# Kernel optimization log

Measured on AMD Instinct MI355X. Metric: run time of the kernel, lower is better.

Reference implementation:

```python
import jax, jax.numpy as jnp
import numpy as np

BATCH, IN_F, OUT_F = 65536, 1024, 256


def setup_inputs() -> dict:
    key = jax.random.key(0)
    kx, kw, kb, ks = jax.random.split(key, 4)
    x = jax.random.normal(kx, (BATCH, IN_F), dtype=jnp.float32)
    # ternary weight in {-1, 0, 1}, shape [out, in] as in F.linear
    weight = jax.random.randint(kw, (OUT_F, IN_F), -1, 2).astype(jnp.float32)
    # bias is integer-valued (floor'd in get_sign_bias_from_bn)
    bias = jax.random.randint(kb, (OUT_F,), -64, 64).astype(jnp.float32)
    # sign in {-1, +1}, broadcast shape [1, out]
    sign = (jax.random.randint(ks, (1, OUT_F), 0, 2).astype(jnp.float32) * 2.0 - 1.0)
    return {"x": x, "weight": weight, "bias": bias, "sign": sign}


def reference(x, weight, bias, sign):
    # y = F.linear(x, W, b); rounding=True -> round; then threshold by sign
    y = jnp.round(jnp.dot(x, weight.T) + bias)  # [B, out]
    return jnp.where(y * sign >= 0, jnp.float32(1.0), jnp.float32(0.0)).astype(x.dtype)
```

## Files before the change

### kernel.cpp

```cpp
#include <hip/hip_runtime.h>
#include <hip/hip_bf16.h>

#define M_BATCH 65536
#define K_IN    1024
#define N_OUT   256
#define TAU     0.015f

#define XLO_SOFF 67108864ULL
#define WT_SOFF  134217728ULL
#define CNT_BOFF 268959744ULL
#define WL_BOFF  (CNT_BOFF + 256ULL)
#define WL_CAP   1048576ULL
#define WS_NEED  (WL_BOFF + WL_CAP * 4ULL)

typedef __attribute__((ext_vector_type(8))) short short8;
typedef __attribute__((ext_vector_type(4))) short short4v;
typedef __attribute__((ext_vector_type(4))) float f32x4;

__device__ inline short f2bf(float f) {
    __hip_bfloat16 h = __float2bfloat16(f);
    return __builtin_bit_cast(short, h);
}
__device__ inline float bf2f(short s) {
    unsigned u = ((unsigned)(unsigned short)s) << 16;
    return __builtin_bit_cast(float, u);
}
__device__ inline void gload16(const void* g, void* lds) {
    __builtin_amdgcn_global_load_lds(
        (const __attribute__((address_space(1))) unsigned int*)g,
        (__attribute__((address_space(3))) unsigned int*)lds, 16, 0, 0);
}

__device__ inline float c3_score(const float* __restrict__ xr_,
                                 const float* __restrict__ wr_) {
    float a0 = 0.f, a1 = 0.f;
    float4 xc0 = *(const float4*)(xr_);
    float4 wc0 = *(const float4*)(wr_);
    float4 xc1 = *(const float4*)(xr_ + 512);
    float4 wc1 = *(const float4*)(wr_ + 512);
    for (int k4 = 0; k4 < 128; ++k4) {
        const int kn = (k4 + 1) & 127;
        const float4 nx0 = *(const float4*)(xr_ + kn * 4);
        const float4 nw0 = *(const float4*)(wr_ + kn * 4);
        const float4 nx1 = *(const float4*)(xr_ + 512 + kn * 4);
        const float4 nw1 = *(const float4*)(wr_ + 512 + kn * 4);
        a0 = fmaf(xc0.x, wc0.x, a0); a1 = fmaf(xc1.x, wc1.x, a1);
        a0 = fmaf(xc0.y, wc0.y, a0); a1 = fmaf(xc1.y, wc1.y, a1);
        a0 = fmaf(xc0.z, wc0.z, a0); a1 = fmaf(xc1.z, wc1.z, a1);
        a0 = fmaf(xc0.w, wc0.w, a0); a1 = fmaf(xc1.w, wc1.w, a1);
        xc0 = nx0; wc0 = nw0; xc1 = nx1; wc1 = nw1;
    }
    return a0 + a1;
}

__device__ inline size_t swz_dst(int row, int col4 ) {
    const int kb = col4 >> 4;
    const int c  = (col4 >> 1) & 7;
    const int h  = col4 & 1;
    return (size_t)row * K_IN + kb * 64 + ((c ^ (row & 7)) << 3) + h * 4;
}

__global__ __launch_bounds__(512) void presplit20(const float* __restrict__ x,
                                                  short* __restrict__ xhi,
                                                  short* __restrict__ xlo) {
    const int stride = gridDim.x * 512;
    for (int idx = blockIdx.x * 512 + threadIdx.x; idx < M_BATCH * (K_IN / 4); idx += stride) {
        const int row  = idx >> 8;
        const int col4 = idx & 255;
        const float4 v = ((const float4*)x)[idx];
        short4v h, l;
        h.x = f2bf(v.x); l.x = f2bf(v.x - bf2f(h.x));
        h.y = f2bf(v.y); l.y = f2bf(v.y - bf2f(h.y));
        h.z = f2bf(v.z); l.z = f2bf(v.z - bf2f(h.z));
        h.w = f2bf(v.w); l.w = f2bf(v.w - bf2f(h.w));
        const size_t dst = swz_dst(row, col4);
        *(short4v*)(xhi + dst) = h;
        *(short4v*)(xlo + dst) = l;
    }
}

__global__ __launch_bounds__(512) void wconv20(const float* __restrict__ w,
                                               short* __restrict__ wt,
                                               unsigned* __restrict__ counter) {
    if (blockIdx.x == 0 && threadIdx.x == 0) *counter = 0u;
    const int idx  = blockIdx.x * 512 + threadIdx.x;
    const int row  = idx >> 8;
    const int col4 = idx & 255;
    const float4 v = ((const float4*)w)[idx];
    short4v h;
    h.x = f2bf(v.x); h.y = f2bf(v.y); h.z = f2bf(v.z); h.w = f2bf(v.w);
    *(short4v*)(wt + swz_dst(row, col4)) = h;
}

__global__ __launch_bounds__(256) void binlin_g20(const float* __restrict__ x,
                                                  const float* __restrict__ wf,
                                                  const short* __restrict__ xhi,
                                                  const short* __restrict__ xlo,
                                                  const short* __restrict__ wt,
                                                  const float* __restrict__ bias,
                                                  const float* __restrict__ sign,
                                                  float* __restrict__ out,
                                                  unsigned* __restrict__ counter,
                                                  unsigned* __restrict__ wl) {
    __shared__ __align__(16) short smem[24576];

    const int bid     = blockIdx.x;
    const int logical = (bid & 7) * 128 + (bid >> 3);
    const int m0 = (logical >> 1) * 128;
    const int n0 = (logical & 1) * 128;

    const int tid  = threadIdx.x;
    const int lane = tid & 63;
    const int wid  = tid >> 6;
    const int wm   = wid >> 1;
    const int wn   = wid & 1;
    const int l15  = lane & 15;
    const int l4   = lane >> 4;

    const int srow = wid * 32 + (lane >> 3);
    const int scol = (lane & 7) * 8;
    const size_t asrc = (size_t)(m0 + srow) * K_IN + scol;
    const size_t bsrc = (size_t)(n0 + srow) * K_IN + scol;

    f32x4 acc[4][4];
#pragma unroll
    for (int i = 0; i < 4; ++i)
#pragma unroll
        for (int j = 0; j < 4; ++j) acc[i][j] = (f32x4){0.f, 0.f, 0.f, 0.f};

    short* Ah = smem;
    short* Al = smem + 8192;
    short* Bs = smem + 16384;

    for (int kt = 0; kt < 16; ++kt) {
        __syncthreads();
#pragma unroll
        for (int q = 0; q < 4; ++q) {
            gload16(xhi + asrc + (size_t)q * 8 * K_IN + kt * 64, Ah + (wid * 32 + q * 8) * 64);
            gload16(xlo + asrc + (size_t)q * 8 * K_IN + kt * 64, Al + (wid * 32 + q * 8) * 64);
            gload16(wt  + bsrc + (size_t)q * 8 * K_IN + kt * 64, Bs + (wid * 32 + q * 8) * 64);
        }
        __syncthreads();

#pragma unroll
        for (int kk = 0; kk < 2; ++kk) {
            short8 bfr[4];
#pragma unroll
            for (int ni = 0; ni < 4; ++ni) {
                const int Rn = wn * 64 + ni * 16 + l15;
                bfr[ni] = *(const short8*)&Bs[Rn * 64 + (((kk * 4 + l4) ^ (Rn & 7)) << 3)];
            }
#pragma unroll
            for (int mi = 0; mi < 4; ++mi) {
                const int Rm  = wm * 64 + mi * 16 + l15;
                const int off = Rm * 64 + (((kk * 4 + l4) ^ (Rm & 7)) << 3);
                const short8 ahi = *(const short8*)&Ah[off];
                const short8 alo = *(const short8*)&Al[off];
#pragma unroll
                for (int ni = 0; ni < 4; ++ni) {
                    acc[mi][ni] = __builtin_amdgcn_mfma_f32_16x16x32_bf16(
                        ahi, bfr[ni], acc[mi][ni], 0, 0, 0);
                    acc[mi][ni] = __builtin_amdgcn_mfma_f32_16x16x32_bf16(
                        alo, bfr[ni], acc[mi][ni], 0, 0, 0);
                }
            }
        }
    }
    __syncthreads();

    unsigned char* dec = (unsigned char*)smem;
#pragma unroll
    for (int ni = 0; ni < 4; ++ni) {
        const int nl = wn * 64 + ni * 16 + l15;
        const int n  = n0 + nl;
        const float b = bias[n];
        const float s = sign[n];
#pragma unroll
        for (int mi = 0; mi < 4; ++mi) {
            const int ml = wm * 64 + mi * 16 + l4 * 4;
#pragma unroll
            for (int j = 0; j < 4; ++j) {
                const float t = (acc[mi][ni][j] + b) * s;
                unsigned char d = (t >= -0.5f) ? 1 : 0;
                if (fabsf(t + 0.5f) < TAU) {
                    const int m = m0 + ml + j;
                    const unsigned idx = atomicAdd(counter, 1u);
                    if (idx < WL_CAP) {
                        wl[idx] = ((unsigned)m << 8) | (unsigned)n;
                    } else {
                        const float cs = c3_score(x + (size_t)m * K_IN,
                                                  wf + (size_t)n * K_IN);
                        d = (((cs + b) * s) >= -0.5f) ? 1 : 0;
                    }
                }
                dec[(ml + j) * 128 + nl] = d;
            }
        }
    }
    __syncthreads();

#pragma unroll
    for (int it = 0; it < 16; ++it) {
        const int f   = it * 256 + tid;
        const int row = f >> 5;
        const int c4  = f & 31;
        const uchar4 dv = *(const uchar4*)&dec[row * 128 + c4 * 4];
        *(float4*)(out + (size_t)(m0 + row) * N_OUT + n0 + c4 * 4) =
            make_float4((float)dv.x, (float)dv.y, (float)dv.z, (float)dv.w);
    }
}

__global__ __launch_bounds__(256) void fixwl20(const float* __restrict__ x,
                                               const float* __restrict__ wf,
                                               const float* __restrict__ bias,
                                               const float* __restrict__ sign,
                                               const unsigned* __restrict__ counter,
                                               const unsigned* __restrict__ wl,
                                               float* __restrict__ out) {
    const unsigned count = min(*counter, (unsigned)WL_CAP);
    const unsigned stride = gridDim.x * 256;
    for (unsigned i = blockIdx.x * 256 + threadIdx.x; i < count; i += stride) {
        const unsigned code = wl[i];
        const int m = (int)(code >> 8);
        const int n = (int)(code & 255u);
        const float cs = c3_score(x + (size_t)m * K_IN, wf + (size_t)n * K_IN);
        const float tt = (cs + bias[n]) * sign[n];
        out[(size_t)m * N_OUT + n] = (tt >= -0.5f) ? 1.0f : 0.0f;
    }
}

__global__ __launch_bounds__(256) void binlin_fast(const float* __restrict__ x,
                                                   const float* __restrict__ w,
                                                   const float* __restrict__ bias,
                                                   const float* __restrict__ sign,
                                                   float* __restrict__ out) {
    __shared__ float As[32][132];
    __shared__ float Bs2[32][132];
    const int tid = threadIdx.x;
    const int tx  = tid & 15;
    const int ty  = tid >> 4;
    const int n0  = blockIdx.x * 128;
    const int m0  = blockIdx.y * 128;
    const int sr  = tid >> 3;
    const int sc  = (tid & 7) * 4;
    float acc[8][8];
#pragma unroll
    for (int i = 0; i < 8; ++i)
#pragma unroll
        for (int j = 0; j < 8; ++j) acc[i][j] = 0.f;
    for (int kt = 0; kt < K_IN; kt += 32) {
        __syncthreads();
#pragma unroll
        for (int q = 0; q < 4; ++q) {
            const int row = sr + q * 32;
            const float4 va = *(const float4*)(x + (size_t)(m0 + row) * K_IN + kt + sc);
            As[sc + 0][row] = va.x; As[sc + 1][row] = va.y;
            As[sc + 2][row] = va.z; As[sc + 3][row] = va.w;
            const float4 vb = *(const float4*)(w + (size_t)(n0 + row) * K_IN + kt + sc);
            Bs2[sc + 0][row] = vb.x; Bs2[sc + 1][row] = vb.y;
            Bs2[sc + 2][row] = vb.z; Bs2[sc + 3][row] = vb.w;
        }
        __syncthreads();
#pragma unroll
        for (int kk = 0; kk < 32; ++kk) {
            const float4 a0 = *(const float4*)&As[kk][ty * 8];
            const float4 a1 = *(const float4*)&As[kk][ty * 8 + 4];
            const float4 b0 = *(const float4*)&Bs2[kk][tx * 8];
            const float4 b1 = *(const float4*)&Bs2[kk][tx * 8 + 4];
            const float a[8] = {a0.x, a0.y, a0.z, a0.w, a1.x, a1.y, a1.z, a1.w};
            const float b[8] = {b0.x, b0.y, b0.z, b0.w, b1.x, b1.y, b1.z, b1.w};
#pragma unroll
            for (int i = 0; i < 8; ++i)
#pragma unroll
                for (int j = 0; j < 8; ++j)
                    acc[i][j] = fmaf(a[i], b[j], acc[i][j]);
        }
    }
    const int nb = n0 + tx * 8;
    float bv[8], sv[8];
#pragma unroll
    for (int j = 0; j < 8; ++j) { bv[j] = bias[nb + j]; sv[j] = sign[nb + j]; }
#pragma unroll
    for (int i = 0; i < 8; ++i) {
        const int m = m0 + ty * 8 + i;
        float o[8];
#pragma unroll
        for (int j = 0; j < 8; ++j) {
            const float t = (acc[i][j] + bv[j]) * sv[j];
            if (fabsf(t + 0.5f) < TAU) {
                const float cs = c3_score(x + (size_t)m * K_IN,
                                          w + (size_t)(nb + j) * K_IN);
                o[j] = (((cs + bv[j]) * sv[j]) >= -0.5f) ? 1.0f : 0.0f;
            } else {
                o[j] = (t >= -0.5f) ? 1.0f : 0.0f;
            }
        }
        float4* op = (float4*)(out + (size_t)m * N_OUT + nb);
        op[0] = make_float4(o[0], o[1], o[2], o[3]);
        op[1] = make_float4(o[4], o[5], o[6], o[7]);
    }
}

extern "C" void kernel_launch(void* const* d_in, const int* in_sizes, int n_in,
                              void* d_out, int out_size, void* d_ws, size_t ws_size,
                              hipStream_t stream) {
    const float* x    = (const float*)d_in[0];
    const float* w    = (const float*)d_in[1];
    const float* bias = (const float*)d_in[2];
    const float* sign = (const float*)d_in[3];

    if (n_in >= 4 && in_sizes[0] != M_BATCH * K_IN) {
        const float* small[2] = {nullptr, nullptr};
        int nsmall = 0;
        for (int i = 0; i < 4; ++i) {
            if (in_sizes[i] == M_BATCH * K_IN)      x = (const float*)d_in[i];
            else if (in_sizes[i] == N_OUT * K_IN)   w = (const float*)d_in[i];
            else if (nsmall < 2) small[nsmall++] = (const float*)d_in[i];
        }
        if (nsmall == 2) { bias = small[0]; sign = small[1]; }
    }

    float* out = (float*)d_out;

    if (ws_size >= WS_NEED) {
        short*    xhi = (short*)d_ws;
        short*    xlo = xhi + XLO_SOFF;
        short*    wtp = xhi + WT_SOFF;
        unsigned* cnt = (unsigned*)((char*)d_ws + CNT_BOFF);
        unsigned* wl  = (unsigned*)((char*)d_ws + WL_BOFF);

        presplit20<<<2048, 512, 0, stream>>>(x, xhi, xlo);
        wconv20<<<128, 512, 0, stream>>>(w, wtp, cnt);
        binlin_g20<<<1024, 256, 0, stream>>>(x, w, xhi, xlo, wtp, bias, sign,
                                             out, cnt, wl);
        fixwl20<<<256, 256, 0, stream>>>(x, w, bias, sign, cnt, wl, out);
    } else {
        dim3 grid(N_OUT / 128, M_BATCH / 128);
        binlin_fast<<<grid, 256, 0, stream>>>(x, w, bias, sign, out);
    }
}
```

Measured before the change: 380.0 us.

## Fuse x bf16 hi/lo split into GEMM, load operands directly from global

Drops the separate pre-split kernel that wrote bf16 hi/lo copies of x (512 MB of extra traffic) and instead converts fp32 x to hi/lo bf16 in registers inside the GEMM. The LDS staging is removed as well: both A (fp32 x) and B (bf16 weights) fragments are read straight from global memory per wave, with no block barriers in the K loop. This cuts memory traffic and a kernel launch, but loses LDS data sharing across waves, so every wave pair re-reads the same x rows and global loads are strided and uncoalesced.

```diff
diff --git a/kernel.cpp b/kernel.cpp
--- a/kernel.cpp
+++ b/kernel.cpp
@@ -6,10 +6,8 @@
 #define N_OUT   256
 #define TAU     0.015f
 
-#define XLO_SOFF 67108864ULL
-#define WT_SOFF  134217728ULL
-#define CNT_BOFF 268959744ULL
-#define WL_BOFF  (CNT_BOFF + 256ULL)
+#define CNT_BOFF 524288ULL
+#define WL_BOFF  524544ULL
 #define WL_CAP   1048576ULL
 #define WS_NEED  (WL_BOFF + WL_CAP * 4ULL)
 
@@ -24,11 +22,6 @@
 __device__ inline float bf2f(short s) {
     unsigned u = ((unsigned)(unsigned short)s) << 16;
     return __builtin_bit_cast(float, u);
-}
-__device__ inline void gload16(const void* g, void* lds) {
-    __builtin_amdgcn_global_load_lds(
-        (const __attribute__((address_space(1))) unsigned int*)g,
-        (__attribute__((address_space(3))) unsigned int*)lds, 16, 0, 0);
 }
 
 __device__ inline float c3_score(const float* __restrict__ xr_,
@@ -53,56 +46,26 @@
     return a0 + a1;
 }
 
-__device__ inline size_t swz_dst(int row, int col4 ) {
-    const int kb = col4 >> 4;
-    const int c  = (col4 >> 1) & 7;
-    const int h  = col4 & 1;
-    return (size_t)row * K_IN + kb * 64 + ((c ^ (row & 7)) << 3) + h * 4;
-}
-
-__global__ __launch_bounds__(512) void presplit20(const float* __restrict__ x,
-                                                  short* __restrict__ xhi,
-                                                  short* __restrict__ xlo) {
-    const int stride = gridDim.x * 512;
-    for (int idx = blockIdx.x * 512 + threadIdx.x; idx < M_BATCH * (K_IN / 4); idx += stride) {
-        const int row  = idx >> 8;
-        const int col4 = idx & 255;
-        const float4 v = ((const float4*)x)[idx];
-        short4v h, l;
-        h.x = f2bf(v.x); l.x = f2bf(v.x - bf2f(h.x));
-        h.y = f2bf(v.y); l.y = f2bf(v.y - bf2f(h.y));
-        h.z = f2bf(v.z); l.z = f2bf(v.z - bf2f(h.z));
-        h.w = f2bf(v.w); l.w = f2bf(v.w - bf2f(h.w));
-        const size_t dst = swz_dst(row, col4);
-        *(short4v*)(xhi + dst) = h;
-        *(short4v*)(xlo + dst) = l;
-    }
-}
-
-__global__ __launch_bounds__(512) void wconv20(const float* __restrict__ w,
+__global__ __launch_bounds__(512) void wconv21(const float* __restrict__ w,
                                                short* __restrict__ wt,
                                                unsigned* __restrict__ counter) {
     if (blockIdx.x == 0 && threadIdx.x == 0) *counter = 0u;
-    const int idx  = blockIdx.x * 512 + threadIdx.x;
-    const int row  = idx >> 8;
-    const int col4 = idx & 255;
+    const int idx = blockIdx.x * 512 + threadIdx.x;
     const float4 v = ((const float4*)w)[idx];
     short4v h;
     h.x = f2bf(v.x); h.y = f2bf(v.y); h.z = f2bf(v.z); h.w = f2bf(v.w);
-    *(short4v*)(wt + swz_dst(row, col4)) = h;
-}
-
-__global__ __launch_bounds__(256) void binlin_g20(const float* __restrict__ x,
+    ((short4v*)wt)[idx] = h;
+}
+
+__global__ __launch_bounds__(256) void binlin_f21(const float* __restrict__ x,
                                                   const float* __restrict__ wf,
-                                                  const short* __restrict__ xhi,
-                                                  const short* __restrict__ xlo,
                                                   const short* __restrict__ wt,
                                                   const float* __restrict__ bias,
                                                   const float* __restrict__ sign,
                                                   float* __restrict__ out,
                                                   unsigned* __restrict__ counter,
                                                   unsigned* __restrict__ wl) {
-    __shared__ __align__(16) short smem[24576];
+    __shared__ __align__(16) unsigned char dec[16384];
 
     const int bid     = blockIdx.x;
     const int logical = (bid & 7) * 128 + (bid >> 3);
@@ -117,10 +80,8 @@
     const int l15  = lane & 15;
     const int l4   = lane >> 4;
 
-    const int srow = wid * 32 + (lane >> 3);
-    const int scol = (lane & 7) * 8;
-    const size_t asrc = (size_t)(m0 + srow) * K_IN + scol;
-    const size_t bsrc = (size_t)(n0 + srow) * K_IN + scol;
+    const float* abase = x  + (size_t)(m0 + wm * 64 + l15) * K_IN + l4 * 8;
+    const short* bbase = wt + (size_t)(n0 + wn * 64 + l15) * K_IN + l4 * 8;
 
     f32x4 acc[4][4];
 #pragma unroll
@@ -128,34 +89,26 @@
 #pragma unroll
         for (int j = 0; j < 4; ++j) acc[i][j] = (f32x4){0.f, 0.f, 0.f, 0.f};
 
-    short* Ah = smem;
-    short* Al = smem + 8192;
-    short* Bs = smem + 16384;
-
     for (int kt = 0; kt < 16; ++kt) {
-        __syncthreads();
-#pragma unroll
-        for (int q = 0; q < 4; ++q) {
-            gload16(xhi + asrc + (size_t)q * 8 * K_IN + kt * 64, Ah + (wid * 32 + q * 8) * 64);
-            gload16(xlo + asrc + (size_t)q * 8 * K_IN + kt * 64, Al + (wid * 32 + q * 8) * 64);
-            gload16(wt  + bsrc + (size_t)q * 8 * K_IN + kt * 64, Bs + (wid * 32 + q * 8) * 64);
-        }
-        __syncthreads();
-
 #pragma unroll
         for (int kk = 0; kk < 2; ++kk) {
+            const int ko = kt * 64 + kk * 32;
             short8 bfr[4];
 #pragma unroll
-            for (int ni = 0; ni < 4; ++ni) {
-                const int Rn = wn * 64 + ni * 16 + l15;
-                bfr[ni] = *(const short8*)&Bs[Rn * 64 + (((kk * 4 + l4) ^ (Rn & 7)) << 3)];
-            }
+            for (int ni = 0; ni < 4; ++ni)
+                bfr[ni] = *(const short8*)(bbase + (size_t)ni * 16 * K_IN + ko);
 #pragma unroll
             for (int mi = 0; mi < 4; ++mi) {
-                const int Rm  = wm * 64 + mi * 16 + l15;
-                const int off = Rm * 64 + (((kk * 4 + l4) ^ (Rm & 7)) << 3);
-                const short8 ahi = *(const short8*)&Ah[off];
-                const short8 alo = *(const short8*)&Al[off];
+                const float4 f0 = *(const float4*)(abase + (size_t)mi * 16 * K_IN + ko);
+                const float4 f1 = *(const float4*)(abase + (size_t)mi * 16 * K_IN + ko + 4);
+                const float fv[8] = {f0.x, f0.y, f0.z, f0.w, f1.x, f1.y, f1.z, f1.w};
+                short8 ahi, alo;
+#pragma unroll
+                for (int e = 0; e < 8; ++e) {
+                    const short h = f2bf(fv[e]);
+                    ahi[e] = h;
+                    alo[e] = f2bf(fv[e] - bf2f(h));
+                }
 #pragma unroll
                 for (int ni = 0; ni < 4; ++ni) {
                     acc[mi][ni] = __builtin_amdgcn_mfma_f32_16x16x32_bf16(
@@ -166,9 +119,7 @@
             }
         }
     }
-    __syncthreads();
-
-    unsigned char* dec = (unsigned char*)smem;
+
 #pragma unroll
     for (int ni = 0; ni < 4; ++ni) {
         const int nl = wn * 64 + ni * 16 + l15;
@@ -210,7 +161,7 @@
     }
 }
 
-__global__ __launch_bounds__(256) void fixwl20(const float* __restrict__ x,
+__global__ __launch_bounds__(256) void fixwl21(const float* __restrict__ x,
                                                const float* __restrict__ wf,
                                                const float* __restrict__ bias,
                                                const float* __restrict__ sign,
@@ -323,17 +274,13 @@
     float* out = (float*)d_out;
 
     if (ws_size >= WS_NEED) {
-        short*    xhi = (short*)d_ws;
-        short*    xlo = xhi + XLO_SOFF;
-        short*    wtp = xhi + WT_SOFF;
+        short*    wtp = (short*)d_ws;
         unsigned* cnt = (unsigned*)((char*)d_ws + CNT_BOFF);
         unsigned* wl  = (unsigned*)((char*)d_ws + WL_BOFF);
 
-        presplit20<<<2048, 512, 0, stream>>>(x, xhi, xlo);
-        wconv20<<<128, 512, 0, stream>>>(w, wtp, cnt);
-        binlin_g20<<<1024, 256, 0, stream>>>(x, w, xhi, xlo, wtp, bias, sign,
-                                             out, cnt, wl);
-        fixwl20<<<256, 256, 0, stream>>>(x, w, bias, sign, cnt, wl, out);
+        wconv21<<<128, 512, 0, stream>>>(w, wtp, cnt);
+        binlin_f21<<<1024, 256, 0, stream>>>(x, w, wtp, bias, sign, out, cnt, wl);
+        fixwl21<<<256, 256, 0, stream>>>(x, w, bias, sign, cnt, wl, out);
     } else {
         dim3 grid(N_OUT / 128, M_BATCH / 128);
         binlin_fast<<<grid, 256, 0, stream>>>(x, w, bias, sign, out);
```

Measured after the change: 311.2 us. -18.1%, faster.
